# Kernel tuning notes

Hardware: AMD Instinct MI355X
Metric: run time of the kernel (lower is better)

Reference implementation:

```python
import jax, jax.numpy as jnp
import numpy as np

NUM_EXPERTS = 8
NUM_LANGS = 4
TOP_K = 2
D_MODEL = 1024
EXPERT_SIZE = 4096
B, S = 2, 2048


def setup_inputs() -> dict:
    key = jax.random.key(0)
    ks = jax.random.split(key, 6)
    def xavier(k, shape, fan_in, fan_out):
        a = float(np.sqrt(6.0 / (fan_in + fan_out)))
        return jax.random.uniform(k, shape, jnp.float32, -a, a)
    return {
        "x": jax.random.normal(ks[0], (B, S, D_MODEL), jnp.float32),
        "router_w": xavier(ks[1], (NUM_EXPERTS, D_MODEL), D_MODEL, NUM_EXPERTS),
        "router_b": jnp.zeros((NUM_EXPERTS,), jnp.float32),
        "lang_w": xavier(ks[2], (NUM_LANGS, D_MODEL), D_MODEL, NUM_LANGS),
        "lang_b": jnp.zeros((NUM_LANGS,), jnp.float32),
        "w1": xavier(ks[3], (NUM_EXPERTS, D_MODEL, EXPERT_SIZE), D_MODEL, EXPERT_SIZE),
        "b1": jnp.zeros((NUM_EXPERTS, EXPERT_SIZE), jnp.float32),
        "w2": xavier(ks[4], (NUM_EXPERTS, EXPERT_SIZE, D_MODEL), EXPERT_SIZE, D_MODEL),
        "b2": jnp.zeros((NUM_EXPERTS, D_MODEL), jnp.float32),
    }


def reference(x, router_w, router_b, lang_w, lang_b, w1, b1, w2, b2):
    # Language-aware routing bias
    lang_logits = x @ lang_w.T + lang_b                      # [B,S,L]
    lang_probs = jax.nn.softmax(lang_logits, axis=-1)
    # lang_probs[..., idx:idx+2].sum(-1): slice may be width 1 at the edge,
    # emulate with a zero pad column.
    lp_pad = jnp.pad(lang_probs, ((0, 0), (0, 0), (0, 1)))
    idx = jnp.arange(NUM_EXPERTS) % NUM_LANGS                # [E]
    expert_weights = lp_pad[..., idx] + lp_pad[..., idx + 1] # [B,S,E]

    router_logits = x @ router_w.T + router_b + 0.1 * expert_weights
    router_probs = jax.nn.softmax(router_logits, axis=-1)   # [B,S,E]
    top_p, top_i = jax.lax.top_k(router_probs, TOP_K)        # [B,S,K]
    top_p = top_p / top_p.sum(axis=-1, keepdims=True)

    # Dense per-expert MLP (dropout=0 / eval). torch GELU default = exact erf.
    h = jax.nn.gelu(jnp.einsum('bsd,edh->bseh', x, w1) + b1, approximate=False)
    expert_out = jnp.einsum('bseh,ehd->bsed', h, w2) + b2    # [B,S,E,D]

    sel = jnp.take_along_axis(expert_out, top_i[..., None], axis=2)  # [B,S,K,D]
    return (top_p[..., None] * sel).sum(axis=2)              # [B,S,D]
```

## Files before the change

kernel.cpp:

```cpp
#include <hip/hip_runtime.h>
#include <cstdint>
#include <cstddef>

#define T_TOK 4096
#define DM 1024
#define HS 4096
#define NE 8
#define MAXROWS 10240
#define MAXTILES 40

typedef __attribute__((ext_vector_type(8))) short short8;
typedef __attribute__((ext_vector_type(4))) float floatx4;

__device__ __forceinline__ unsigned short f2bf(float f) {
  union { float f; unsigned u; } v; v.f = f;
  unsigned r = (v.u + 0x7fffu + ((v.u >> 16) & 1u)) >> 16;
  return (unsigned short)r;
}

__device__ __forceinline__ void gload_lds16(const void* g, void* l) {
  __builtin_amdgcn_global_load_lds((const __attribute__((address_space(1))) void*)g,
                                   (__attribute__((address_space(3))) void*)l, 16, 0, 0);
}


__global__ void k_cvt_init(const float* __restrict__ x, unsigned short* __restrict__ xb,
                           int* counts, int* cursor, unsigned* list) {
  int i = blockIdx.x * 256 + threadIdx.x;
  if (i < NE) { counts[i] = 0; cursor[i] = 0; }
  if (i < MAXROWS) list[i] = 0xFFFFFFFFu;
  float4 v = ((const float4*)x)[i];
  union { unsigned short us[4]; uint2 u2; } o;
  o.us[0] = f2bf(v.x); o.us[1] = f2bf(v.y); o.us[2] = f2bf(v.z); o.us[3] = f2bf(v.w);
  ((uint2*)xb)[i] = o.u2;
}

__global__ void k_route(const float* __restrict__ x, const float* __restrict__ rw,
                        const float* __restrict__ rb, const float* __restrict__ lw,
                        const float* __restrict__ lb, int* __restrict__ top_i,
                        float* __restrict__ top_p, int* __restrict__ counts) {
  int t = blockIdx.x * 4 + (threadIdx.x >> 6);
  int lane = threadIdx.x & 63;
  const float4* xt = (const float4*)(x + (size_t)t * DM);
  float4 xv[4];
#pragma unroll
  for (int j = 0; j < 4; j++) xv[j] = xt[lane * 4 + j];
  float dots[12];
#pragma unroll
  for (int r = 0; r < 12; r++) {
    const float4* wr = (const float4*)(r < 4 ? lw + r * DM : rw + (r - 4) * DM);
    float s = 0.f;
#pragma unroll
    for (int j = 0; j < 4; j++) {
      float4 w = wr[lane * 4 + j];
      s += xv[j].x * w.x + xv[j].y * w.y + xv[j].z * w.z + xv[j].w * w.w;
    }
#pragma unroll
    for (int o = 32; o > 0; o >>= 1) s += __shfl_xor(s, o, 64);
    dots[r] = s;
  }
  if (lane == 0) {
    float lp[4]; float m = -1e30f;
#pragma unroll
    for (int i = 0; i < 4; i++) { lp[i] = dots[i] + lb[i]; m = fmaxf(m, lp[i]); }
    float sum = 0.f;
#pragma unroll
    for (int i = 0; i < 4; i++) { lp[i] = expf(lp[i] - m); sum += lp[i]; }
#pragma unroll
    for (int i = 0; i < 4; i++) lp[i] /= sum;
    float ew[4];
    ew[0] = lp[0] + lp[1]; ew[1] = lp[1] + lp[2]; ew[2] = lp[2] + lp[3]; ew[3] = lp[3];
    float r8[8];
#pragma unroll
    for (int e = 0; e < 8; e++) r8[e] = dots[4 + e] + rb[e] + 0.1f * ew[e & 3];
    int e0 = 0;
#pragma unroll
    for (int e = 1; e < 8; e++) if (r8[e] > r8[e0]) e0 = e;
    int e1 = (e0 == 0) ? 1 : 0;
#pragma unroll
    for (int e = 0; e < 8; e++) if (e != e0 && r8[e] > r8[e1]) e1 = e;
    float tt = expf(r8[e1] - r8[e0]);
    float w0 = 1.f / (1.f + tt);
    float w1 = tt / (1.f + tt);
    top_i[t * 2] = e0; top_i[t * 2 + 1] = e1;
    top_p[t * 2] = w0; top_p[t * 2 + 1] = w1;
    atomicAdd(&counts[e0], 1); atomicAdd(&counts[e1], 1);
  }
}

__global__ void k_offsets(const int* counts, int* off) {
  if (threadIdx.x == 0) {
    int acc = 0;
    for (int e = 0; e < NE; e++) {
      off[e] = acc;
      int p = ((counts[e] + 255) >> 8) << 8;
      acc += p;
    }
    off[NE] = acc;
  }
}

__global__ void k_scatter(const int* __restrict__ top_i, const int* __restrict__ off,
                          int* cursor, unsigned* __restrict__ list) {
  int t = blockIdx.x * 256 + threadIdx.x;
  if (t >= T_TOK) return;
#pragma unroll
  for (int k = 0; k < 2; k++) {
    int e = top_i[t * 2 + k];
    int pos = atomicAdd(&cursor[e], 1);
    list[off[e] + pos] = (unsigned)(t * 2 + k);
  }
}

__global__ void k_transpose_bf16(const float* __restrict__ src, unsigned short* __restrict__ dst,
                                 int K, int N) {
  __shared__ float tile[64][65];
  const float* s = src + (size_t)blockIdx.z * K * N;
  unsigned short* d = dst + (size_t)blockIdx.z * K * N;
  int n0 = blockIdx.x * 64, k0 = blockIdx.y * 64;
  int tr = threadIdx.x >> 4;
  int tc = (threadIdx.x & 15) * 4;
#pragma unroll
  for (int j = 0; j < 4; j++) {
    int row = tr + j * 16;
    float4 v = *(const float4*)&s[(size_t)(k0 + row) * N + n0 + tc];
    tile[row][tc + 0] = v.x; tile[row][tc + 1] = v.y;
    tile[row][tc + 2] = v.z; tile[row][tc + 3] = v.w;
  }
  __syncthreads();
#pragma unroll
  for (int j = 0; j < 4; j++) {
    int n = tr + j * 16;
    union { unsigned short us[4]; uint2 u2; } o;
#pragma unroll
    for (int i = 0; i < 4; i++) o.us[i] = f2bf(tile[tc + i][n]);
    *(uint2*)&d[(size_t)(n0 + n) * K + k0 + tc] = o.u2;
  }
}

__global__ void k_init_out(const int* __restrict__ top_i, const float* __restrict__ top_p,
                           const float* __restrict__ b2, float* __restrict__ out) {
  int i = blockIdx.x * 256 + threadIdx.x;
  int t = i >> 10, d = i & 1023;
  int e0 = top_i[t * 2], e1 = top_i[t * 2 + 1];
  out[i] = top_p[t * 2] * b2[e0 * DM + d] + top_p[t * 2 + 1] * b2[e1 * DM + d];
}

template <int MODE, int K, int N, int KT>
__global__ __launch_bounds__(512, 1) void k_gemm(
    const unsigned short* __restrict__ Abase,
    const unsigned short* __restrict__ Wt,
    const int* __restrict__ off, const unsigned* __restrict__ list,
    const float* __restrict__ bias, const float* __restrict__ top_p,
    unsigned short* __restrict__ Hout, float* __restrict__ out) {
  int gx = gridDim.x, gy = gridDim.y;
  int flat = (blockIdx.z * gy + blockIdx.y) * gx + blockIdx.x;
  int nwg = gx * gy * gridDim.z;
  int cpx = nwg >> 3;
  int swz = (flat & 7) * cpx + (flat >> 3);
  int bn = swz % gx; int rest = swz / gx;
  int bm = rest % gy; int z = rest / gy;
  int n0 = bn * 256, r0 = bm * 256;
  int kb = z * (KT * 64);
  int total = off[NE];
  if (r0 >= total) return;
  int e = 0;
  while (r0 >= off[e + 1]) ++e;

  __shared__ __align__(16) unsigned short lA[2][256 * 64];
  __shared__ __align__(16) unsigned short lB[2][256 * 64];
  __shared__ float sP[256];
  __shared__ int sTok[256];

  int tid = threadIdx.x;
  int w = tid >> 6, lane = tid & 63;
  int g8 = lane >> 3, c8 = lane & 7;
  int rowS = w * 8 + g8;
  int koff = (c8 ^ g8) * 8;

  unsigned aOff[4], bOff[4];
#pragma unroll
  for (int l = 0; l < 4; l++) {
    int rowA = l * 64 + rowS;
    unsigned arow;
    if (MODE == 0) {
      unsigned pair = list[r0 + rowA];
      arow = (pair == 0xFFFFFFFFu) ? 0u : (pair >> 1);
    } else {
      arow = (unsigned)(r0 + rowA);
    }
    aOff[l] = arow * (unsigned)K + (unsigned)(kb + koff);
    bOff[l] = (unsigned)(e * N + n0 + rowA) * (unsigned)K + (unsigned)(kb + koff);
  }
  int ldsb = rowS * 64 + c8 * 8;

  if (MODE == 1 && tid < 256) {
    unsigned pair = list[r0 + tid];
    if (pair == 0xFFFFFFFFu) { sTok[tid] = -1; sP[tid] = 0.f; }
    else { sTok[tid] = (int)(pair >> 1); sP[tid] = top_p[pair]; }
  }

  int wm = w >> 2, wn = w & 3;
  int lr = lane & 15, kq = lane >> 4;
  int rsel = (lr & 7);

  floatx4 acc[8][4] = {};

#define STAGE(BUF, TT)                                                        \
  do {                                                                        \
    _Pragma("unroll")                                                         \
    for (int l = 0; l < 4; l++)                                               \
      gload_lds16(Abase + aOff[l] + (TT) * 64, &lA[BUF][l * 4096 + ldsb]);    \
    _Pragma("unroll")                                                         \
    for (int l = 0; l < 4; l++)                                               \
      gload_lds16(Wt + bOff[l] + (TT) * 64, &lB[BUF][l * 4096 + ldsb]);       \
  } while (0)

  __syncthreads();
  STAGE(0, 0);
  asm volatile("s_waitcnt vmcnt(0)" ::: "memory");
  __builtin_amdgcn_s_barrier();

  int cur = 0;
  for (int t = 0; t < KT; ++t) {
    const short8* qA = (const short8*)lA[cur];
    const short8* qB = (const short8*)lB[cur];
    short8 a[8], b[4];
#pragma unroll
    for (int m = 0; m < 8; m++)
      a[m] = qA[(wm * 128 + m * 16 + lr) * 8 + ((0 * 4 + kq) ^ rsel)];
#pragma unroll
    for (int n = 0; n < 4; n++)
      b[n] = qB[(wn * 64 + n * 16 + lr) * 8 + ((0 * 4 + kq) ^ rsel)];
    if (t + 1 < KT) STAGE(cur ^ 1, t + 1);
    __builtin_amdgcn_s_setprio(1);
#pragma unroll
    for (int m = 0; m < 8; m++)
#pragma unroll
      for (int n = 0; n < 4; n++)
        acc[m][n] = __builtin_amdgcn_mfma_f32_16x16x32_bf16(a[m], b[n], acc[m][n], 0, 0, 0);
    __builtin_amdgcn_s_setprio(0);
#pragma unroll
    for (int m = 0; m < 8; m++)
      a[m] = qA[(wm * 128 + m * 16 + lr) * 8 + ((1 * 4 + kq) ^ rsel)];
#pragma unroll
    for (int n = 0; n < 4; n++)
      b[n] = qB[(wn * 64 + n * 16 + lr) * 8 + ((1 * 4 + kq) ^ rsel)];
    __builtin_amdgcn_s_setprio(1);
#pragma unroll
    for (int m = 0; m < 8; m++)
#pragma unroll
      for (int n = 0; n < 4; n++)
        acc[m][n] = __builtin_amdgcn_mfma_f32_16x16x32_bf16(a[m], b[n], acc[m][n], 0, 0, 0);
    __builtin_amdgcn_s_setprio(0);
    asm volatile("s_waitcnt vmcnt(0)" ::: "memory");
    __builtin_amdgcn_s_barrier();
    cur ^= 1;
  }
#undef STAGE

  if (MODE == 0) {
    float bcol[4];
#pragma unroll
    for (int n = 0; n < 4; n++) bcol[n] = bias[e * N + n0 + wn * 64 + n * 16 + lr];
#pragma unroll
    for (int m = 0; m < 8; m++)
#pragma unroll
      for (int n = 0; n < 4; n++)
#pragma unroll
        for (int g = 0; g < 4; g++) {
          int row = wm * 128 + m * 16 + kq * 4 + g;
          int col = wn * 64 + n * 16 + lr;
          float v = acc[m][n][g] + bcol[n];
          float u = v * (0.7978845608f + 0.0356774081f * v * v);
          float gl = v / (1.f + __expf(-2.f * u));
          Hout[(size_t)(r0 + row) * (size_t)N + n0 + col] = f2bf(gl);
        }
  } else {
#pragma unroll
    for (int m = 0; m < 8; m++)
#pragma unroll
      for (int g = 0; g < 4; g++) {
        int row = wm * 128 + m * 16 + kq * 4 + g;
        int tok = sTok[row];
        if (tok >= 0) {
          float p = sP[row];
#pragma unroll
          for (int n = 0; n < 4; n++) {
            int col = wn * 64 + n * 16 + lr;
            atomicAdd(&out[(size_t)tok * DM + n0 + col], p * acc[m][n][g]);
          }
        }
      }
  }
}


extern "C" void kernel_launch(void* const* d_in, const int* in_sizes, int n_in,
                              void* d_out, int out_size, void* d_ws, size_t ws_size,
                              hipStream_t stream) {
  const float* x  = (const float*)d_in[0];
  const float* rw = (const float*)d_in[1];
  const float* rb = (const float*)d_in[2];
  const float* lw = (const float*)d_in[3];
  const float* lb = (const float*)d_in[4];
  const float* w1 = (const float*)d_in[5];
  const float* b1 = (const float*)d_in[6];
  const float* w2 = (const float*)d_in[7];
  const float* b2 = (const float*)d_in[8];
  float* out = (float*)d_out;
  char* ws = (char*)d_ws;

  int* counts = (int*)ws;
  int* cursor = (int*)(ws + 32);
  int* off    = (int*)(ws + 64);
  int* top_i  = (int*)(ws + 128);
  float* top_p = (float*)(ws + 128 + 32768);
  unsigned* list = (unsigned*)(ws + 128 + 65536);
  unsigned short* xb = (unsigned short*)(ws + 131072);
  unsigned short* wt = (unsigned short*)(ws + 131072 + 8388608);
  unsigned short* h  = (unsigned short*)(ws + 131072 + 8388608 + 67108864);

  k_cvt_init<<<dim3(T_TOK * DM / 4 / 256), dim3(256), 0, stream>>>(x, xb, counts, cursor, list);
  k_route<<<dim3(T_TOK / 4), dim3(256), 0, stream>>>(x, rw, rb, lw, lb, top_i, top_p, counts);
  k_offsets<<<dim3(1), dim3(64), 0, stream>>>(counts, off);
  k_scatter<<<dim3(T_TOK / 256), dim3(256), 0, stream>>>(top_i, off, cursor, list);
  k_transpose_bf16<<<dim3(HS / 64, DM / 64, NE), dim3(256), 0, stream>>>(w1, wt, DM, HS);
  k_init_out<<<dim3(T_TOK * DM / 256), dim3(256), 0, stream>>>(top_i, top_p, b2, out);
  k_gemm<0, DM, HS, DM / 64><<<dim3(HS / 256, MAXTILES, 1), dim3(512), 0, stream>>>(
      xb, wt, off, list, b1, top_p, h, nullptr);
  k_transpose_bf16<<<dim3(DM / 64, HS / 64, NE), dim3(256), 0, stream>>>(w2, wt, HS, DM);
  k_gemm<1, HS, DM, HS / 4 / 64><<<dim3(DM / 256, MAXTILES, 4), dim3(512), 0, stream>>>(
      h, wt, off, list, nullptr, top_p, nullptr, out);
}
```

Measured before the change: 531.2 us.

## Restructure GEMM main loop into four-phase ping-pong with split staged loads

Splits each K-tile iteration of the expert GEMM into four quadrant MFMA phases separated by barriers, loading A/B fragments per quadrant instead of all at once. Global-to-LDS staging is split into half-tile chunks issued between phases, with a deeper prefetch (B two tiles ahead) and partial vmcnt waits instead of a full drain. The goal is to overlap memory traffic with MFMA work and cut register pressure from the fragments, at the cost of more barriers and intricate buffer-hazard reasoning.

Result: slower. 566.4 us (+6.6%).

```diff
diff --git a/kernel.cpp b/kernel.cpp
--- a/kernel.cpp
+++ b/kernel.cpp
@@ -22,6 +22,8 @@
   __builtin_amdgcn_global_load_lds((const __attribute__((address_space(1))) void*)g,
                                    (__attribute__((address_space(3))) void*)l, 16, 0, 0);
 }
+
+#define BAR() asm volatile("s_barrier" ::: "memory")
 
 
 __global__ void k_cvt_init(const float* __restrict__ x, unsigned short* __restrict__ xb,
@@ -202,62 +204,115 @@
 
   int wm = w >> 2, wn = w & 3;
   int lr = lane & 15, kq = lane >> 4;
-  int rsel = (lr & 7);
+  int rsel = lr & 7;
 
   floatx4 acc[8][4] = {};
 
-#define STAGE(BUF, TT)                                                        \
+#define STAGE_A_H(BUF, TT, H)                                                 \
   do {                                                                        \
-    _Pragma("unroll")                                                         \
-    for (int l = 0; l < 4; l++)                                               \
-      gload_lds16(Abase + aOff[l] + (TT) * 64, &lA[BUF][l * 4096 + ldsb]);    \
-    _Pragma("unroll")                                                         \
-    for (int l = 0; l < 4; l++)                                               \
-      gload_lds16(Wt + bOff[l] + (TT) * 64, &lB[BUF][l * 4096 + ldsb]);       \
+    gload_lds16(Abase + aOff[2 * (H)] + (TT) * 64,                            \
+                &lA[BUF][(2 * (H)) * 4096 + ldsb]);                           \
+    gload_lds16(Abase + aOff[2 * (H) + 1] + (TT) * 64,                        \
+                &lA[BUF][(2 * (H) + 1) * 4096 + ldsb]);                       \
   } while (0)
+#define STAGE_B_H(BUF, TT, H)                                                 \
+  do {                                                                        \
+    gload_lds16(Wt + bOff[2 * (H)] + (TT) * 64,                               \
+                &lB[BUF][(2 * (H)) * 4096 + ldsb]);                           \
+    gload_lds16(Wt + bOff[2 * (H) + 1] + (TT) * 64,                           \
+                &lB[BUF][(2 * (H) + 1) * 4096 + ldsb]);                       \
+  } while (0)
 
   __syncthreads();
-  STAGE(0, 0);
-  asm volatile("s_waitcnt vmcnt(0)" ::: "memory");
-  __builtin_amdgcn_s_barrier();
-
-  int cur = 0;
+
+  STAGE_A_H(0, 0, 0); STAGE_A_H(0, 0, 1);
+  STAGE_B_H(0, 0, 0); STAGE_B_H(0, 0, 1);
+  STAGE_B_H(1, 1, 0); STAGE_B_H(1, 1, 1);
+  STAGE_A_H(1, 1, 0);
+  asm volatile("s_waitcnt vmcnt(6)" ::: "memory");
+  BAR();
+
+  int curb = 0;
   for (int t = 0; t < KT; ++t) {
-    const short8* qA = (const short8*)lA[cur];
-    const short8* qB = (const short8*)lB[cur];
-    short8 a[8], b[4];
-#pragma unroll
-    for (int m = 0; m < 8; m++)
-      a[m] = qA[(wm * 128 + m * 16 + lr) * 8 + ((0 * 4 + kq) ^ rsel)];
-#pragma unroll
-    for (int n = 0; n < 4; n++)
-      b[n] = qB[(wn * 64 + n * 16 + lr) * 8 + ((0 * 4 + kq) ^ rsel)];
-    if (t + 1 < KT) STAGE(cur ^ 1, t + 1);
+    const short8* qA = (const short8*)lA[curb];
+    const short8* qB = (const short8*)lB[curb];
+    short8 a[4][2], b0[2][2], b1[2][2];
+#pragma unroll
+    for (int m = 0; m < 4; m++)
+#pragma unroll
+      for (int kk = 0; kk < 2; kk++)
+        a[m][kk] = qA[(wm * 128 + m * 16 + lr) * 8 + ((kk * 4 + kq) ^ rsel)];
+#pragma unroll
+    for (int n = 0; n < 2; n++)
+#pragma unroll
+      for (int kk = 0; kk < 2; kk++)
+        b0[n][kk] = qB[(wn * 64 + n * 16 + lr) * 8 + ((kk * 4 + kq) ^ rsel)];
+    if (t + 1 < KT) STAGE_A_H(curb ^ 1, t + 1, 1);
+    BAR();
     __builtin_amdgcn_s_setprio(1);
 #pragma unroll
-    for (int m = 0; m < 8; m++)
-#pragma unroll
-      for (int n = 0; n < 4; n++)
-        acc[m][n] = __builtin_amdgcn_mfma_f32_16x16x32_bf16(a[m], b[n], acc[m][n], 0, 0, 0);
+    for (int m = 0; m < 4; m++)
+#pragma unroll
+      for (int n = 0; n < 2; n++)
+#pragma unroll
+        for (int kk = 0; kk < 2; kk++)
+          acc[m][n] = __builtin_amdgcn_mfma_f32_16x16x32_bf16(a[m][kk], b0[n][kk], acc[m][n], 0, 0, 0);
     __builtin_amdgcn_s_setprio(0);
-#pragma unroll
-    for (int m = 0; m < 8; m++)
-      a[m] = qA[(wm * 128 + m * 16 + lr) * 8 + ((1 * 4 + kq) ^ rsel)];
-#pragma unroll
-    for (int n = 0; n < 4; n++)
-      b[n] = qB[(wn * 64 + n * 16 + lr) * 8 + ((1 * 4 + kq) ^ rsel)];
+    BAR();
+#pragma unroll
+    for (int n = 0; n < 2; n++)
+#pragma unroll
+      for (int kk = 0; kk < 2; kk++)
+        b1[n][kk] = qB[(wn * 64 + 32 + n * 16 + lr) * 8 + ((kk * 4 + kq) ^ rsel)];
+    BAR();
     __builtin_amdgcn_s_setprio(1);
 #pragma unroll
-    for (int m = 0; m < 8; m++)
-#pragma unroll
-      for (int n = 0; n < 4; n++)
-        acc[m][n] = __builtin_amdgcn_mfma_f32_16x16x32_bf16(a[m], b[n], acc[m][n], 0, 0, 0);
+    for (int m = 0; m < 4; m++)
+#pragma unroll
+      for (int n = 0; n < 2; n++)
+#pragma unroll
+        for (int kk = 0; kk < 2; kk++)
+          acc[m][n + 2] = __builtin_amdgcn_mfma_f32_16x16x32_bf16(a[m][kk], b1[n][kk], acc[m][n + 2], 0, 0, 0);
     __builtin_amdgcn_s_setprio(0);
-    asm volatile("s_waitcnt vmcnt(0)" ::: "memory");
-    __builtin_amdgcn_s_barrier();
-    cur ^= 1;
-  }
-#undef STAGE
+    BAR();
+#pragma unroll
+    for (int m = 0; m < 4; m++)
+#pragma unroll
+      for (int kk = 0; kk < 2; kk++)
+        a[m][kk] = qA[(wm * 128 + 64 + m * 16 + lr) * 8 + ((kk * 4 + kq) ^ rsel)];
+    if (t + 2 < KT) STAGE_B_H(curb, t + 2, 0);
+    BAR();
+    __builtin_amdgcn_s_setprio(1);
+#pragma unroll
+    for (int m = 0; m < 4; m++)
+#pragma unroll
+      for (int n = 0; n < 2; n++)
+#pragma unroll
+        for (int kk = 0; kk < 2; kk++)
+          acc[m + 4][n] = __builtin_amdgcn_mfma_f32_16x16x32_bf16(a[m][kk], b0[n][kk], acc[m + 4][n], 0, 0, 0);
+    __builtin_amdgcn_s_setprio(0);
+    BAR();
+    if (t + 2 < KT) {
+      STAGE_B_H(curb, t + 2, 1);
+      STAGE_A_H(curb, t + 2, 0);
+      asm volatile("s_waitcnt vmcnt(6)" ::: "memory");
+    } else {
+      asm volatile("s_waitcnt vmcnt(0)" ::: "memory");
+    }
+    BAR();
+    __builtin_amdgcn_s_setprio(1);
+#pragma unroll
+    for (int m = 0; m < 4; m++)
+#pragma unroll
+      for (int n = 0; n < 2; n++)
+#pragma unroll
+        for (int kk = 0; kk < 2; kk++)
+          acc[m + 4][n + 2] = __builtin_amdgcn_mfma_f32_16x16x32_bf16(a[m][kk], b1[n][kk], acc[m + 4][n + 2], 0, 0, 0);
+    __builtin_amdgcn_s_setprio(0);
+    curb ^= 1;
+  }
+#undef STAGE_A_H
+#undef STAGE_B_H
 
   if (MODE == 0) {
     float bcol[4];
```
